# Performance work log

Hardware: AMD Instinct MI355X
Metric: run time of the kernel (lower is better)

Reference implementation:

```python
import jax, jax.numpy as jnp
import numpy as np

WH, WW = 8, 8          # window size
DIM = 384
HEADS = 12
N = WH * WW            # tokens per window = 64


def _relative_position_index():
    ch, cw = np.meshgrid(np.arange(WH), np.arange(WW), indexing='ij')
    coords = np.stack([ch, cw]).reshape(2, -1)            # (2, N)
    rel = coords[:, :, None] - coords[:, None, :]         # (2, N, N)
    rel = rel.transpose(1, 2, 0).astype(np.int32)         # (N, N, 2)
    rel[:, :, 0] += WH - 1
    rel[:, :, 1] += WW - 1
    rel[:, :, 0] *= 2 * WW - 1
    return jnp.asarray(rel.sum(-1))                       # (N, N) int32


def setup_inputs() -> dict:
    key = jax.random.key(0)
    ks = jax.random.split(key, 6)
    B_ = 4096
    x = jax.random.normal(ks[0], (B_, N, DIM), dtype=jnp.float32)
    mask = jnp.zeros((B_, N, N), dtype=jnp.float32)       # nW == B_ here (B=1)
    qkv_w = jax.random.normal(ks[1], (DIM, 3 * DIM), dtype=jnp.float32) * 0.02
    qkv_b = jnp.zeros((3 * DIM,), dtype=jnp.float32)
    rpb_table = jax.random.normal(ks[2], ((2 * WH - 1) * (2 * WW - 1), HEADS), dtype=jnp.float32) * 0.02
    proj_w = jax.random.normal(ks[3], (DIM, DIM), dtype=jnp.float32) * 0.02
    proj_b = jnp.zeros((DIM,), dtype=jnp.float32)
    rpi = _relative_position_index()
    return {"x": x, "mask": mask, "qkv_w": qkv_w, "qkv_b": qkv_b,
            "rpb_table": rpb_table, "proj_w": proj_w, "proj_b": proj_b, "rpi": rpi}


def reference(x, mask, qkv_w, qkv_b, rpb_table, proj_w, proj_b, rpi):
    B_, n, C = x.shape
    hd = C // HEADS
    scale = hd ** -0.5
    qkv = (x @ qkv_w + qkv_b).reshape(B_, n, 3, HEADS, hd)
    q, k, v = qkv[:, :, 0], qkv[:, :, 1], qkv[:, :, 2]    # (B_, n, H, hd)
    attn = jnp.einsum('bnhd,bmhd->bhnm', q * scale, k)    # (B_, H, n, n)
    bias = rpb_table[rpi]                                 # (n, n, H)
    attn = attn + jnp.transpose(bias, (2, 0, 1))[None]    # add rel-pos bias
    nW = mask.shape[0]
    attn = attn.reshape(B_ // nW, nW, HEADS, n, n) + mask[None, :, None]
    attn = attn.reshape(B_, HEADS, n, n)
    attn = jax.nn.softmax(attn, axis=-1)
    out = jnp.einsum('bhnm,bmhd->bnhd', attn, v).reshape(B_, n, C)
    return out @ proj_w + proj_b
```

## Files before the change

### kernel.cpp

```cpp
#include <hip/hip_runtime.h>
#include <hip/hip_bf16.h>

typedef unsigned short u16;
typedef unsigned int   u32;
typedef __attribute__((ext_vector_type(8))) __bf16 bf16x8;
typedef __attribute__((ext_vector_type(4))) float  f32x4;

#define NWIN   4096
#define SEQ    64
#define DIMC   384
#define NHEAD  12
#define HDIM   32
#define NROWS  262144
#define NQKV   1152

__device__ __forceinline__ u16 f2bf(float f){
  u32 x = __float_as_uint(f);
  return (u16)((x + 0x7fffu + ((x >> 16) & 1u)) >> 16);
}

__device__ __forceinline__ void gload_lds16(const u16* g, u16* l){
  __builtin_amdgcn_global_load_lds(
      (const __attribute__((address_space(1))) void*)g,
      (__attribute__((address_space(3))) void*)l, 16, 0, 0);
}

__device__ __forceinline__ f32x4 mfma_bf16(bf16x8 a, bf16x8 b, f32x4 c){
  return __builtin_amdgcn_mfma_f32_16x16x32_bf16(a, b, c, 0, 0, 0);
}

__global__ void prep_x(const float* __restrict__ x, u16* __restrict__ xb){
  size_t i = ((size_t)blockIdx.x * 256 + threadIdx.x) * 8;
  f32x4 a = *(const f32x4*)(x + i);
  f32x4 b = *(const f32x4*)(x + i + 4);
  union { u16 u[8]; bf16x8 v; } o;
  #pragma unroll
  for(int j=0;j<4;j++) o.u[j]   = f2bf(a[j]);
  #pragma unroll
  for(int j=0;j<4;j++) o.u[4+j] = f2bf(b[j]);
  *(bf16x8*)(xb + i) = o.v;
}

__global__ void prep_w(const float* __restrict__ qw, const float* __restrict__ pw,
                       const float* __restrict__ rpb, const int* __restrict__ rpi,
                       u16* __restrict__ wqT, u16* __restrict__ wpT,
                       float* __restrict__ biasT){
  int id = blockIdx.x * 256 + threadIdx.x;
  if (id < NQKV*DIMC){
    int n = id / DIMC, k = id % DIMC;
    wqT[id] = f2bf(qw[(size_t)k*NQKV + n]);
  } else if (id < NQKV*DIMC + DIMC*DIMC){
    int j = id - NQKV*DIMC;
    int n = j / DIMC, k = j % DIMC;
    wpT[j] = f2bf(pw[(size_t)k*DIMC + n]);
  } else {
    int j = id - (NQKV*DIMC + DIMC*DIMC);
    int h = j / 4096, nm = j % 4096;
    biasT[j] = rpb[rpi[nm]*NHEAD + h];
  }
}

template<int NB, int EPI>
__global__ __launch_bounds__(256, 2) void gemm_bt(
    const u16* __restrict__ A, const u16* __restrict__ Bt,
    const float* __restrict__ bias,
    u16* __restrict__ oq, u16* __restrict__ okk, u16* __restrict__ ov,
    float* __restrict__ of)
{
  __shared__ u16 Al[2][8192];
  __shared__ u16 Bl[2][8192];
  const int bid = blockIdx.x;
  const int bm = bid / NB, bn = bid % NB;
  const size_t m0 = (size_t)bm * 128;
  const int n0 = bn * 128;
  const int tid = threadIdx.x, wv = tid >> 6, ln = tid & 63;
  const int wr = wv >> 1, wc = wv & 1;
  const int cl = ln & 15, q8 = ln >> 4;

  f32x4 acc[4][4];
  const f32x4 zero4 = {0.f,0.f,0.f,0.f};
  #pragma unroll
  for(int i=0;i<4;i++)
    #pragma unroll
    for(int j=0;j<4;j++) acc[i][j] = zero4;

  auto stage = [&](int bufi, int kt){
    #pragma unroll
    for(int c=0;c<4;c++){
      int un  = (wv*4+c)*64 + ln;
      int row = un >> 3;
      int u   = (un & 7) ^ (row & 7);
      gload_lds16(A  + (m0 + row)*DIMC + kt*64 + u*8, &Al[bufi][(wv*4+c)*512]);
      gload_lds16(Bt + (size_t)(n0 + row)*DIMC + kt*64 + u*8, &Bl[bufi][(wv*4+c)*512]);
    }
  };

  stage(0, 0);
  #pragma unroll
  for(int kt=0;kt<6;kt++){
    const int bufi = kt & 1;
    __syncthreads();
    if (kt < 5) stage(bufi^1, kt+1);
    #pragma unroll
    for(int ks=0;ks<2;ks++){
      bf16x8 af[4], bfr[4];
      #pragma unroll
      for(int i=0;i<4;i++){
        int row = wr*64 + i*16 + cl;
        int u = (ks*4 + q8) ^ (row & 7);
        af[i] = *(const bf16x8*)&Al[bufi][row*64 + u*8];
      }
      #pragma unroll
      for(int j=0;j<4;j++){
        int row = wc*64 + j*16 + cl;
        int u = (ks*4 + q8) ^ (row & 7);
        bfr[j] = *(const bf16x8*)&Bl[bufi][row*64 + u*8];
      }
      #pragma unroll
      for(int i=0;i<4;i++)
        #pragma unroll
        for(int j=0;j<4;j++)
          acc[i][j] = mfma_bf16(af[i], bfr[j], acc[i][j]);
    }
  }

  float bj[4];
  #pragma unroll
  for(int j=0;j<4;j++) bj[j] = bias[n0 + wc*64 + j*16 + cl];

  if (EPI == 0){
    const int t = n0 / DIMC;
    const int lc0 = n0 - t*DIMC + wc*64 + cl;
    u16* dst = (t==0) ? oq : (t==1) ? okk : ov;
    #pragma unroll
    for(int i=0;i<4;i++){
      size_t r0 = m0 + wr*64 + i*16 + q8*4;
      #pragma unroll
      for(int j=0;j<4;j++)
        #pragma unroll
        for(int r=0;r<4;r++)
          dst[(r0 + r)*DIMC + lc0 + j*16] = f2bf(acc[i][j][r] + bj[j]);
    }
  } else {
    const int lc0 = n0 + wc*64 + cl;
    #pragma unroll
    for(int i=0;i<4;i++){
      size_t r0 = m0 + wr*64 + i*16 + q8*4;
      #pragma unroll
      for(int j=0;j<4;j++)
        #pragma unroll
        for(int r=0;r<4;r++)
          of[(r0 + r)*DIMC + lc0 + j*16] = acc[i][j][r] + bj[j];
    }
  }
}

__global__ __launch_bounds__(256, 1) void attn_win(
    const u16* __restrict__ Q, const u16* __restrict__ K, const u16* __restrict__ V,
    const float* __restrict__ biasT, const float* __restrict__ mask,
    u16* __restrict__ AO)
{
  __shared__ u16 qk[NHEAD][4096];
  __shared__ u16 vt[NHEAD][2048];
  const int w = blockIdx.x;
  const int tid = threadIdx.x, wv = tid >> 6, ln = tid & 63;
  const int cl = ln & 15, g = ln >> 4;
  const size_t rb = (size_t)w * SEQ;
  const f32x4 zero4 = {0.f,0.f,0.f,0.f};

  #pragma unroll
  for(int c=0;c<12;c++){
    int f = wv*12 + c;
    int h = f >> 2, i = f & 3;
    size_t src = (rb + i*16 + (ln>>2))*DIMC + h*HDIM + (ln&3)*8;
    gload_lds16(Q + src, &qk[h][i*512]);
    gload_lds16(K + src, &qk[h][2048 + i*512]);
  }
  #pragma unroll
  for(int c=0;c<12;c++){
    int ch = c*256 + tid;
    int tok = ch / 48, dc = ch % 48;
    union { bf16x8 v; u16 u[8]; } vv;
    vv.v = *(const bf16x8*)(V + (rb + tok)*DIMC + dc*8);
    #pragma unroll
    for(int j=0;j<8;j++){
      int d = dc*8 + j, h = d >> 5, dh = d & 31;
      vt[h][dh*64 + (((tok>>3) ^ (dh&7)) * 8) + (tok & 7)] = vv.u[j];
    }
  }
  __syncthreads();

  const float scale = 0.17677669529663687f;
  #pragma unroll 1
  for(int c=0;c<3;c++){
    const int h = wv*3 + c;
    u16* ph = qk[h];
    bf16x8 aq[4], bk[4];
    #pragma unroll
    for(int i=0;i<4;i++) aq[i] = *(const bf16x8*)&ph[(i*16 + cl)*32 + g*8];
    #pragma unroll
    for(int j=0;j<4;j++) bk[j] = *(const bf16x8*)&ph[2048 + (j*16 + cl)*32 + g*8];
    f32x4 S[4][4];
    #pragma unroll
    for(int i=0;i<4;i++)
      #pragma unroll
      for(int j=0;j<4;j++)
        S[i][j] = mfma_bf16(aq[i], bk[j], zero4);

    float l[4][4];
    #pragma unroll
    for(int i=0;i<4;i++){
      #pragma unroll
      for(int r=0;r<4;r++){
        int row = i*16 + g*4 + r;
        float v0[4];
        #pragma unroll
        for(int j=0;j<4;j++){
          int col2 = j*16 + cl;
          v0[j] = S[i][j][r]*scale + biasT[h*4096 + row*64 + col2]
                                   + mask[(size_t)w*4096 + row*64 + col2];
        }
        float mx = fmaxf(fmaxf(v0[0],v0[1]), fmaxf(v0[2],v0[3]));
        #pragma unroll
        for(int s=1;s<16;s<<=1) mx = fmaxf(mx, __shfl_xor(mx, s));
        float sm = 0.f;
        #pragma unroll
        for(int j=0;j<4;j++){ v0[j] = __expf(v0[j]-mx); sm += v0[j]; }
        #pragma unroll
        for(int s=1;s<16;s<<=1) sm += __shfl_xor(sm, s);
        l[i][r] = sm;
        #pragma unroll
        for(int j=0;j<4;j++){
          int col2 = j*16 + cl;
          ph[row*64 + (((col2>>3) ^ (row&7))*8) + (col2&7)] = f2bf(v0[j]);
        }
      }
    }
    f32x4 O[4][2];
    #pragma unroll
    for(int i=0;i<4;i++){ O[i][0] = zero4; O[i][1] = zero4; }
    #pragma unroll
    for(int ks=0;ks<2;ks++){
      bf16x8 ap[4], bv[2];
      #pragma unroll
      for(int i=0;i<4;i++){
        int m = i*16 + cl;
        ap[i] = *(const bf16x8*)&ph[m*64 + (((ks*4+g) ^ (m&7))*8)];
      }
      #pragma unroll
      for(int j=0;j<2;j++){
        int n = j*16 + cl;
        bv[j] = *(const bf16x8*)&vt[h][n*64 + (((ks*4+g) ^ (n&7))*8)];
      }
      #pragma unroll
      for(int i=0;i<4;i++)
        #pragma unroll
        for(int j=0;j<2;j++)
          O[i][j] = mfma_bf16(ap[i], bv[j], O[i][j]);
    }
    #pragma unroll
    for(int i=0;i<4;i++){
      #pragma unroll
      for(int r=0;r<4;r++){
        float inv = 1.0f / l[i][r];
        size_t orow = (rb + i*16 + g*4 + r)*DIMC + h*HDIM;
        AO[orow + cl]      = f2bf(O[i][0][r]*inv);
        AO[orow + 16 + cl] = f2bf(O[i][1][r]*inv);
      }
    }
  }
}

extern "C" void kernel_launch(void* const* d_in, const int* in_sizes, int n_in,
                              void* d_out, int out_size, void* d_ws, size_t ws_size,
                              hipStream_t stream) {
  const float* x      = (const float*)d_in[0];
  const float* mask   = (const float*)d_in[1];
  const float* qkv_w  = (const float*)d_in[2];
  const float* qkv_b  = (const float*)d_in[3];
  const float* rpb    = (const float*)d_in[4];
  const float* proj_w = (const float*)d_in[5];
  const float* proj_b = (const float*)d_in[6];
  const int*   rpi    = (const int*)d_in[7];

  u16* xb  = (u16*)d_ws;
  u16* vb  = xb + (size_t)NROWS*DIMC;
  u16* wqT = vb + (size_t)NROWS*DIMC;
  u16* wpT = wqT + (size_t)NQKV*DIMC;
  float* biasT = (float*)(wpT + (size_t)DIMC*DIMC);
  u16* qb = (u16*)d_out;
  u16* kb = qb + (size_t)NROWS*DIMC;
  u16* ao = xb;

  prep_x<<<(NROWS*(size_t)DIMC)/(256*8), 256, 0, stream>>>(x, xb);
  prep_w<<<(NQKV*DIMC + DIMC*DIMC + NHEAD*4096)/256, 256, 0, stream>>>(
      qkv_w, proj_w, rpb, rpi, wqT, wpT, biasT);
  gemm_bt<9,0><<<2048*9, 256, 0, stream>>>(xb, wqT, qkv_b, qb, kb, vb, nullptr);
  attn_win<<<NWIN, 256, 0, stream>>>(qb, kb, vb, biasT, mask, ao);
  gemm_bt<3,1><<<2048*3, 256, 0, stream>>>(ao, wpT, proj_b, nullptr, nullptr, nullptr,
                                           (float*)d_out);
}
```

Baseline: 1.891 ms.

## Split window attention blocks across head groups to cut LDS and raise occupancy

The attention kernel now launches three blocks per window, each handling four heads with one head per wave. Previously one block processed all twelve heads in a loop. Per-block LDS drops from the full twelve-head Q/K/V staging to a four-head slice, and launch bounds allow three blocks per CU. The aim is better latency hiding through higher occupancy and overlap of the global-to-LDS loads with compute. The cost is that the mask is re-read once per head group and there are more, smaller blocks.

```diff
diff --git a/kernel.cpp b/kernel.cpp
--- a/kernel.cpp
+++ b/kernel.cpp
@@ -155,118 +155,119 @@
   }
 }
 
-__global__ __launch_bounds__(256, 1) void attn_win(
+__global__ __launch_bounds__(256, 3) void attn_win(
     const u16* __restrict__ Q, const u16* __restrict__ K, const u16* __restrict__ V,
     const float* __restrict__ biasT, const float* __restrict__ mask,
     u16* __restrict__ AO)
 {
-  __shared__ u16 qk[NHEAD][4096];
-  __shared__ u16 vt[NHEAD][2048];
-  const int w = blockIdx.x;
+  __shared__ u16 qk[4][4096];
+  __shared__ u16 vt[4][2048];
+  const int bid = blockIdx.x;
+  const int w  = bid / 3, hg = bid % 3;
   const int tid = threadIdx.x, wv = tid >> 6, ln = tid & 63;
   const int cl = ln & 15, g = ln >> 4;
   const size_t rb = (size_t)w * SEQ;
+  const int h0 = hg * 4;
   const f32x4 zero4 = {0.f,0.f,0.f,0.f};
 
   #pragma unroll
-  for(int c=0;c<12;c++){
-    int f = wv*12 + c;
-    int h = f >> 2, i = f & 3;
-    size_t src = (rb + i*16 + (ln>>2))*DIMC + h*HDIM + (ln&3)*8;
-    gload_lds16(Q + src, &qk[h][i*512]);
-    gload_lds16(K + src, &qk[h][2048 + i*512]);
-  }
-  #pragma unroll
-  for(int c=0;c<12;c++){
+  for(int c=0;c<4;c++){
+    int f = wv*4 + c;
+    int hl = f >> 2, i = f & 3;
+    size_t src = (rb + i*16 + (ln>>2))*DIMC + (h0+hl)*HDIM + (ln&3)*8;
+    gload_lds16(Q + src, &qk[hl][i*512]);
+    gload_lds16(K + src, &qk[hl][2048 + i*512]);
+  }
+  #pragma unroll
+  for(int c=0;c<4;c++){
     int ch = c*256 + tid;
-    int tok = ch / 48, dc = ch % 48;
+    int tok = ch >> 4, dc = ch & 15;
     union { bf16x8 v; u16 u[8]; } vv;
-    vv.v = *(const bf16x8*)(V + (rb + tok)*DIMC + dc*8);
+    vv.v = *(const bf16x8*)(V + (rb + tok)*DIMC + h0*HDIM + dc*8);
     #pragma unroll
     for(int j=0;j<8;j++){
-      int d = dc*8 + j, h = d >> 5, dh = d & 31;
-      vt[h][dh*64 + (((tok>>3) ^ (dh&7)) * 8) + (tok & 7)] = vv.u[j];
+      int d = dc*8 + j, hl = d >> 5, dh = d & 31;
+      vt[hl][dh*64 + (((tok>>3) ^ (dh&7)) * 8) + (tok & 7)] = vv.u[j];
     }
   }
   __syncthreads();
 
   const float scale = 0.17677669529663687f;
-  #pragma unroll 1
-  for(int c=0;c<3;c++){
-    const int h = wv*3 + c;
-    u16* ph = qk[h];
-    bf16x8 aq[4], bk[4];
-    #pragma unroll
-    for(int i=0;i<4;i++) aq[i] = *(const bf16x8*)&ph[(i*16 + cl)*32 + g*8];
-    #pragma unroll
-    for(int j=0;j<4;j++) bk[j] = *(const bf16x8*)&ph[2048 + (j*16 + cl)*32 + g*8];
-    f32x4 S[4][4];
+  const int h = h0 + wv;
+  u16* ph = qk[wv];
+  const u16* pv = vt[wv];
+
+  bf16x8 aq[4], bk[4];
+  #pragma unroll
+  for(int i=0;i<4;i++) aq[i] = *(const bf16x8*)&ph[(i*16 + cl)*32 + g*8];
+  #pragma unroll
+  for(int j=0;j<4;j++) bk[j] = *(const bf16x8*)&ph[2048 + (j*16 + cl)*32 + g*8];
+  f32x4 S[4][4];
+  #pragma unroll
+  for(int i=0;i<4;i++)
+    #pragma unroll
+    for(int j=0;j<4;j++)
+      S[i][j] = mfma_bf16(aq[i], bk[j], zero4);
+
+  float l[4][4];
+  #pragma unroll
+  for(int i=0;i<4;i++){
+    #pragma unroll
+    for(int r=0;r<4;r++){
+      int row = i*16 + g*4 + r;
+      float v0[4];
+      #pragma unroll
+      for(int j=0;j<4;j++){
+        int col2 = j*16 + cl;
+        v0[j] = S[i][j][r]*scale + biasT[h*4096 + row*64 + col2]
+                                 + mask[(size_t)w*4096 + row*64 + col2];
+      }
+      float mx = fmaxf(fmaxf(v0[0],v0[1]), fmaxf(v0[2],v0[3]));
+      #pragma unroll
+      for(int s=1;s<16;s<<=1) mx = fmaxf(mx, __shfl_xor(mx, s));
+      float sm = 0.f;
+      #pragma unroll
+      for(int j=0;j<4;j++){ v0[j] = __expf(v0[j]-mx); sm += v0[j]; }
+      #pragma unroll
+      for(int s=1;s<16;s<<=1) sm += __shfl_xor(sm, s);
+      l[i][r] = sm;
+      #pragma unroll
+      for(int j=0;j<4;j++){
+        int col2 = j*16 + cl;
+        ph[row*64 + (((col2>>3) ^ (row&7))*8) + (col2&7)] = f2bf(v0[j]);
+      }
+    }
+  }
+  f32x4 O[4][2];
+  #pragma unroll
+  for(int i=0;i<4;i++){ O[i][0] = zero4; O[i][1] = zero4; }
+  #pragma unroll
+  for(int ks=0;ks<2;ks++){
+    bf16x8 ap[4], bv[2];
+    #pragma unroll
+    for(int i=0;i<4;i++){
+      int m = i*16 + cl;
+      ap[i] = *(const bf16x8*)&ph[m*64 + (((ks*4+g) ^ (m&7))*8)];
+    }
+    #pragma unroll
+    for(int j=0;j<2;j++){
+      int n = j*16 + cl;
+      bv[j] = *(const bf16x8*)&pv[n*64 + (((ks*4+g) ^ (n&7))*8)];
+    }
     #pragma unroll
     for(int i=0;i<4;i++)
       #pragma unroll
-      for(int j=0;j<4;j++)
-        S[i][j] = mfma_bf16(aq[i], bk[j], zero4);
-
-    float l[4][4];
-    #pragma unroll
-    for(int i=0;i<4;i++){
-      #pragma unroll
-      for(int r=0;r<4;r++){
-        int row = i*16 + g*4 + r;
-        float v0[4];
-        #pragma unroll
-        for(int j=0;j<4;j++){
-          int col2 = j*16 + cl;
-          v0[j] = S[i][j][r]*scale + biasT[h*4096 + row*64 + col2]
-                                   + mask[(size_t)w*4096 + row*64 + col2];
-        }
-        float mx = fmaxf(fmaxf(v0[0],v0[1]), fmaxf(v0[2],v0[3]));
-        #pragma unroll
-        for(int s=1;s<16;s<<=1) mx = fmaxf(mx, __shfl_xor(mx, s));
-        float sm = 0.f;
-        #pragma unroll
-        for(int j=0;j<4;j++){ v0[j] = __expf(v0[j]-mx); sm += v0[j]; }
-        #pragma unroll
-        for(int s=1;s<16;s<<=1) sm += __shfl_xor(sm, s);
-        l[i][r] = sm;
-        #pragma unroll
-        for(int j=0;j<4;j++){
-          int col2 = j*16 + cl;
-          ph[row*64 + (((col2>>3) ^ (row&7))*8) + (col2&7)] = f2bf(v0[j]);
-        }
-      }
-    }
-    f32x4 O[4][2];
-    #pragma unroll
-    for(int i=0;i<4;i++){ O[i][0] = zero4; O[i][1] = zero4; }
-    #pragma unroll
-    for(int ks=0;ks<2;ks++){
-      bf16x8 ap[4], bv[2];
-      #pragma unroll
-      for(int i=0;i<4;i++){
-        int m = i*16 + cl;
-        ap[i] = *(const bf16x8*)&ph[m*64 + (((ks*4+g) ^ (m&7))*8)];
-      }
-      #pragma unroll
-      for(int j=0;j<2;j++){
-        int n = j*16 + cl;
-        bv[j] = *(const bf16x8*)&vt[h][n*64 + (((ks*4+g) ^ (n&7))*8)];
-      }
-      #pragma unroll
-      for(int i=0;i<4;i++)
-        #pragma unroll
-        for(int j=0;j<2;j++)
-          O[i][j] = mfma_bf16(ap[i], bv[j], O[i][j]);
-    }
-    #pragma unroll
-    for(int i=0;i<4;i++){
-      #pragma unroll
-      for(int r=0;r<4;r++){
-        float inv = 1.0f / l[i][r];
-        size_t orow = (rb + i*16 + g*4 + r)*DIMC + h*HDIM;
-        AO[orow + cl]      = f2bf(O[i][0][r]*inv);
-        AO[orow + 16 + cl] = f2bf(O[i][1][r]*inv);
-      }
+      for(int j=0;j<2;j++)
+        O[i][j] = mfma_bf16(ap[i], bv[j], O[i][j]);
+  }
+  #pragma unroll
+  for(int i=0;i<4;i++){
+    #pragma unroll
+    for(int r=0;r<4;r++){
+      float inv = 1.0f / l[i][r];
+      size_t orow = (rb + i*16 + g*4 + r)*DIMC + h*HDIM;
+      AO[orow + cl]      = f2bf(O[i][0][r]*inv);
+      AO[orow + 16 + cl] = f2bf(O[i][1][r]*inv);
     }
   }
 }
@@ -296,7 +297,7 @@
   prep_w<<<(NQKV*DIMC + DIMC*DIMC + NHEAD*4096)/256, 256, 0, stream>>>(
       qkv_w, proj_w, rpb, rpi, wqT, wpT, biasT);
   gemm_bt<9,0><<<2048*9, 256, 0, stream>>>(xb, wqT, qkv_b, qb, kb, vb, nullptr);
-  attn_win<<<NWIN, 256, 0, stream>>>(qb, kb, vb, biasT, mask, ao);
+  attn_win<<<NWIN*3, 256, 0, stream>>>(qb, kb, vb, biasT, mask, ao);
   gemm_bt<3,1><<<2048*3, 256, 0, stream>>>(ao, wpT, proj_b, nullptr, nullptr, nullptr,
                                            (float*)d_out);
 }
```

After: 1.613 ms. 1.17x faster.
